# Kernel optimization log

Hardware: AMD Instinct MI355X
Metric: run time of the kernel (lower is better)

The kernel has to match this reference:

```python
import jax, jax.numpy as jnp
import numpy as np

B, T, H, W, C = 8, 16, 64, 64, 16
HID = 64  # hidden_dim of each ConvLSTM cell
K = 3     # kernel size


def _convlstm_step(x, h, c, Wk, b):
    # conv over concat([x, h]) -> 4*HID gate channels (i, f, o, g)
    z = jax.lax.conv_general_dilated(
        jnp.concatenate([x, h], axis=-1), Wk,
        window_strides=(1, 1), padding='SAME',
        dimension_numbers=('NHWC', 'HWIO', 'NHWC')) + b
    i, f, o, g = jnp.split(z, 4, axis=-1)
    c_new = jax.nn.sigmoid(f) * c + jax.nn.sigmoid(i) * jnp.tanh(g)
    h_new = jax.nn.sigmoid(o) * jnp.tanh(c_new)
    return h_new, c_new


def setup_inputs() -> dict:
    key = jax.random.key(0)
    k1, k2, k3 = jax.random.split(key, 3)
    enc_input = jax.random.normal(k1, (B, T, H, W, C), jnp.float32)
    # input cell: in_channels = C + HID; stacked hidden cell: 2*HID
    W0 = jax.random.normal(k2, (K, K, C + HID, 4 * HID), jnp.float32) * 0.05
    b0 = jnp.zeros((4 * HID,), jnp.float32)
    W1 = jax.random.normal(k3, (K, K, 2 * HID, 4 * HID), jnp.float32) * 0.05
    b1 = jnp.zeros((4 * HID,), jnp.float32)
    return {"enc_input": enc_input, "W0": W0, "b0": b0, "W1": W1, "b1": b1}


def reference(enc_input, W0, b0, W1, b1):
    Bv, Tv, Hv, Wv, _ = enc_input.shape
    z0 = jnp.zeros((Bv, Hv, Wv, HID), enc_input.dtype)

    def step(carry, x_t):
        h0, c0, h1, c1 = carry
        h0, c0 = _convlstm_step(x_t, h0, c0, W0, b0)   # input ConvLSTM
        h1, c1 = _convlstm_step(h0, h1, c1, W1, b1)    # stacked hidden ConvLSTM
        return (h0, c0, h1, c1), None

    xs = jnp.moveaxis(enc_input, 1, 0)  # [T, B, H, W, C]
    (h0, c0, h1, c1), _ = jax.lax.scan(step, (z0, z0, z0, z0), xs)
    # Encoder returns last hidden layer's (h, c)
    return (h1, c1)
```

## Files before the change

kernel.cpp:

```cpp
#include <hip/hip_runtime.h>
#include <hip/hip_bf16.h>

#define Bv 8
#define Tv 16
#define Hv 64
#define Wv 64
#define Cv 16
#define HID 64
#define PH 66

typedef short short8 __attribute__((ext_vector_type(8)));
typedef float f32x4 __attribute__((ext_vector_type(4)));
typedef unsigned short u16x8 __attribute__((ext_vector_type(8)));

__device__ __forceinline__ unsigned short f2bf(float x) {
  union { float f; unsigned int u; } v; v.f = x;
  unsigned int r = v.u + 0x7FFF + ((v.u >> 16) & 1);
  return (unsigned short)(r >> 16);
}
__device__ __forceinline__ float sigmoid_f(float x) {
  return 1.f / (1.f + __expf(-x));
}
__device__ __forceinline__ float tanh_f(float x) {
  float e = __expf(2.f * x);
  return 1.f - 2.f / (e + 1.f);
}

__global__ void relayout_w0(const float* __restrict__ W0, unsigned short* __restrict__ out) {
  int o = blockIdx.x * 256 + threadIdx.x;
  if (o >= 27 * 8192) return;
  int cc = o >> 13, t = o & 8191;
  int wn = t >> 11, t2 = t & 2047;
  int g = t2 >> 9, t3 = t2 & 511;
  int l = t3 >> 3, e = t3 & 7;
  int kg = l >> 4, r = l & 15;
  int k = kg * 8 + e;
  int col = g * 64 + wn * 16 + r;
  int tap = cc / 3, cgi = cc - tap * 3;
  int p = cgi * 32 + k;
  float v = 0.f;
  if (p < 16)        v = W0[(size_t)(tap * 80 + p) * 256 + col];
  else if (p >= 32)  v = W0[(size_t)(tap * 80 + (p - 16)) * 256 + col];
  out[o] = f2bf(v);
}
__global__ void relayout_w1(const float* __restrict__ W1, unsigned short* __restrict__ out) {
  int o = blockIdx.x * 256 + threadIdx.x;
  if (o >= 36 * 8192) return;
  int cc = o >> 13, t = o & 8191;
  int wn = t >> 11, t2 = t & 2047;
  int g = t2 >> 9, t3 = t2 & 511;
  int l = t3 >> 3, e = t3 & 7;
  int kg = l >> 4, r = l & 15;
  int k = kg * 8 + e;
  int col = g * 64 + wn * 16 + r;
  int tap = cc >> 2, cgi = cc & 3;
  out[o] = f2bf(W1[(size_t)(tap * 128 + cgi * 32 + k) * 256 + col]);
}

__global__ void zero_init(unsigned short* __restrict__ h0a, unsigned short* __restrict__ h0b,
                          unsigned short* __restrict__ h1a, unsigned short* __restrict__ h1b,
                          unsigned short* __restrict__ xb) {
  int idx = blockIdx.x * 256 + threadIdx.x;
  u16x8 z = {};
  const int XB_CH = (Bv * PH * PH * 32 * 2 * 2) / 16;
  if (idx < XB_CH) { *(u16x8*)(xb + idx * 8) = z; return; }
  idx -= XB_CH;
  int bufi = idx / 16640;
  if (bufi >= 4) return;
  int rem = idx - bufi * 16640;
  int b = rem / 2080, r2 = rem - b * 2080;
  int hp = r2 >> 3, c8 = r2 & 7;
  int y, x;
  if (hp < 66)       { y = 0;  x = hp; }
  else if (hp < 132) { y = 65; x = hp - 66; }
  else { int i2 = hp - 132; y = 1 + (i2 >> 1); x = (i2 & 1) * 65; }
  unsigned short* base = (bufi == 0) ? h0a : (bufi == 1) ? h0b : (bufi == 2) ? h1a : h1b;
  *(u16x8*)(base + ((size_t)((b * PH + y) * PH) + x) * 64 + c8 * 8) = z;
}

__global__ void convert_x0(const float* __restrict__ enc, unsigned short* __restrict__ xb) {
  int idx = blockIdx.x * 256 + threadIdx.x;
  int b = idx >> 12, pix = idx & 4095;
  int y = pix >> 6, x = pix & 63;
  const float* s = enc + ((size_t)(b * Tv + 0) * 4096 + pix) * 16;
  float4 f0 = *(const float4*)(s);
  float4 f1 = *(const float4*)(s + 4);
  float4 f2 = *(const float4*)(s + 8);
  float4 f3 = *(const float4*)(s + 12);
  u16x8 o0, o1;
  o0[0]=f2bf(f0.x); o0[1]=f2bf(f0.y); o0[2]=f2bf(f0.z); o0[3]=f2bf(f0.w);
  o0[4]=f2bf(f1.x); o0[5]=f2bf(f1.y); o0[6]=f2bf(f1.z); o0[7]=f2bf(f1.w);
  o1[0]=f2bf(f2.x); o1[1]=f2bf(f2.y); o1[2]=f2bf(f2.z); o1[3]=f2bf(f2.w);
  o1[4]=f2bf(f3.x); o1[5]=f2bf(f3.y); o1[6]=f2bf(f3.z); o1[7]=f2bf(f3.w);
  unsigned short* d = xb + ((size_t)((b * PH + y + 1) * PH) + (x + 1)) * 32;
  *(u16x8*)(d)     = o0;
  *(u16x8*)(d + 8) = o1;
}

template<int CELL, int NC>
__device__ __forceinline__ void cell_run(
    const char* __restrict__ A0, const char* __restrict__ A1,
    const char* __restrict__ Wr, const float* __restrict__ bias,
    float* __restrict__ cbuf, unsigned short* __restrict__ hout,
    float* __restrict__ h1fin, float* __restrict__ c1fin,
    char* lds, int b, int by, int bx, int tid)
{
  constexpr bool T0C = (CELL == 0) ? (NC == 9) : (NC == 18);
  const int l = tid & 63, w = tid >> 6;
  const int wm = w >> 2, wn = w & 3;
  const int r = l & 15, kg = l >> 4;
  const int j = wn * 16 + r;

  int pixs;
  {
    int ps = w * 16 + r;
    int ys = by * 16 + (ps >> 3), xs = bx * 8 + (ps & 7);
    pixs = (b * PH + ys) * PH + xs;
  }

  auto ISSUE = [&](int cc, int buf) {
    char* dst = lds + buf * 24576;
    int tap, cgi, wcc;
    if (CELL == 0) {
      if (T0C) { tap = cc; cgi = 0; wcc = cc * 3; }
      else     { tap = cc / 3; cgi = cc - tap * 3; wcc = cc; }
    } else {
      if (T0C) { tap = cc >> 1; cgi = cc & 1; wcc = tap * 4 + cgi; }
      else     { tap = cc >> 2; cgi = cc & 3; wcc = cc; }
    }
    int ky = tap / 3, kx = tap - ky * 3;
    const char* srcb;
    unsigned aoff;
    if (CELL == 0) {
      if (cgi == 0) { srcb = A0; aoff = (unsigned)((pixs + ky * PH + kx) * 64 + kg * 16); }
      else { srcb = A1;
             aoff = (unsigned)((pixs + ky * PH + kx) * 128 + ((cgi == 2) ? 64 : 0) + kg * 16); }
    } else {
      srcb = (cgi < 2) ? A0 : A1;
      aoff = (unsigned)((pixs + ky * PH + kx) * 128 + (cgi & 1) * 64 + kg * 16);
    }
    __builtin_amdgcn_global_load_lds((const unsigned int*)(srcb + aoff),
                                     (unsigned int*)(dst + w * 1024), 16, 0, 0);
    const char* wp = Wr + (size_t)wcc * 16384 + (unsigned)(w * 2048 + l * 16);
    __builtin_amdgcn_global_load_lds((const unsigned int*)(wp),
                                     (unsigned int*)(dst + 8192 + w * 2048), 16, 0, 0);
    __builtin_amdgcn_global_load_lds((const unsigned int*)(wp + 1024),
                                     (unsigned int*)(dst + 8192 + w * 2048 + 1024), 16, 0, 0);
  };

  f32x4 acc[4][4] = {};
  short8 af[4], bfv[4];

  ISSUE(0, 0); ISSUE(1, 1);
#pragma unroll
  for (int cc = 0; cc < NC; ++cc) {
    if (cc <= NC - 2) { asm volatile("s_waitcnt vmcnt(3)" ::: "memory"); }
    else              { asm volatile("s_waitcnt vmcnt(0)" ::: "memory"); }
    __builtin_amdgcn_sched_barrier(0);
    __builtin_amdgcn_s_barrier();
    __builtin_amdgcn_sched_barrier(0);

    const char* bufp = lds + (cc % 3) * 24576;
#pragma unroll
    for (int mi = 0; mi < 4; ++mi)
      af[mi] = *(const short8*)(bufp + (wm * 4 + mi) * 1024 + l * 16);
#pragma unroll
    for (int g = 0; g < 4; ++g)
      bfv[g] = *(const short8*)(bufp + 8192 + (wn * 4 + g) * 1024 + l * 16);

    asm volatile("s_waitcnt lgkmcnt(0)" ::: "memory");
    __builtin_amdgcn_sched_barrier(0);
    if (cc + 2 < NC) ISSUE(cc + 2, (cc + 2) % 3);
    __builtin_amdgcn_sched_barrier(0);

#pragma unroll
    for (int mi = 0; mi < 4; ++mi)
#pragma unroll
      for (int g = 0; g < 4; ++g)
        acc[mi][g] = __builtin_amdgcn_mfma_f32_16x16x32_bf16(
            af[mi], bfv[g], acc[mi][g], 0, 0, 0);
  }

  float bi[4];
#pragma unroll
  for (int g = 0; g < 4; ++g) bi[g] = bias[g * 64 + j];
  float cpre[4][4];
#pragma unroll
  for (int mi = 0; mi < 4; ++mi) {
#pragma unroll
    for (int rg = 0; rg < 4; ++rg) {
      if constexpr (T0C) { cpre[mi][rg] = 0.f; }
      else {
        int p = wm * 64 + mi * 16 + kg * 4 + rg;
        int y = by * 16 + (p >> 3), x = bx * 8 + (p & 7);
        cpre[mi][rg] = cbuf[((size_t)((b * Hv + y) * Wv) + x) * HID + j];
      }
    }
  }
#pragma unroll
  for (int mi = 0; mi < 4; ++mi) {
#pragma unroll
    for (int rg = 0; rg < 4; ++rg) {
      int p = wm * 64 + mi * 16 + kg * 4 + rg;
      int y = by * 16 + (p >> 3), x = bx * 8 + (p & 7);
      float zi = acc[mi][0][rg] + bi[0];
      float zf = acc[mi][1][rg] + bi[1];
      float zo = acc[mi][2][rg] + bi[2];
      float zg = acc[mi][3][rg] + bi[3];
      float cn = sigmoid_f(zf) * cpre[mi][rg] + sigmoid_f(zi) * tanh_f(zg);
      float hn = sigmoid_f(zo) * tanh_f(cn);
      size_t ci = ((size_t)((b * Hv + y) * Wv) + x) * HID + j;
      cbuf[ci] = cn;
      hout[((size_t)((b * PH + y + 1) * PH) + (x + 1)) * HID + j] = f2bf(hn);
      if (CELL == 1 && h1fin != nullptr) {
        h1fin[ci] = hn;
        c1fin[ci] = cn;
      }
    }
  }
}

template<int NC1, int NC0, bool LAST>
__global__ __launch_bounds__(512, 4)
void step_fused(const unsigned short* __restrict__ xbr, unsigned short* __restrict__ xbw,
                const unsigned short* __restrict__ h0r, unsigned short* __restrict__ h0w,
                const unsigned short* __restrict__ h1r, unsigned short* __restrict__ h1w,
                const unsigned short* __restrict__ w0r, const unsigned short* __restrict__ w1r,
                const float* __restrict__ b0, const float* __restrict__ b1,
                float* __restrict__ c0, float* __restrict__ c1,
                float* __restrict__ h1f, float* __restrict__ c1f,
                const float* __restrict__ enc, int tnext)
{
  extern __shared__ char lds[];
  const int tid = threadIdx.x;
  const int gid = blockIdx.x;
  int isC1, k;
  if constexpr (NC1 > 0 && NC0 > 0) { isC1 = gid & 1; k = gid >> 1; }
  else if constexpr (NC1 > 0)       { isC1 = 1; k = gid; }
  else                              { isC1 = 0; k = gid; }
  const int b = k >> 5, rem = k & 31;
  const int by = rem >> 3, bx = rem & 7;

  if constexpr (NC1 > 0) {
    if (isC1) {
      cell_run<1, NC1>((const char*)h0r, (const char*)h1r, (const char*)w1r, b1,
                       c1, h1w, LAST ? h1f : nullptr, LAST ? c1f : nullptr,
                       lds, b, by, bx, tid);
      return;
    }
  }
  if constexpr (NC0 > 0) {
    cell_run<0, NC0>((const char*)xbr, (const char*)h0r, (const char*)w0r, b0,
                     c0, h0w, nullptr, nullptr, lds, b, by, bx, tid);
    if (tnext >= 0) {
      int pp = tid >> 2, q4 = tid & 3;
      int y = by * 16 + (pp >> 3), x = bx * 8 + (pp & 7);
      const float* s = enc + ((size_t)(b * Tv + tnext) * 4096 + (y * 64 + x)) * 16 + q4 * 4;
      float4 f = *(const float4*)s;
      unsigned short* d = xbw + ((size_t)((b * PH + y + 1) * PH) + (x + 1)) * 32 + q4 * 4;
      d[0] = f2bf(f.x); d[1] = f2bf(f.y); d[2] = f2bf(f.z); d[3] = f2bf(f.w);
    }
  }
}

extern "C" void kernel_launch(void* const* d_in, const int* in_sizes, int n_in,
                              void* d_out, int out_size, void* d_ws, size_t ws_size,
                              hipStream_t stream) {
  const float* enc = (const float*)d_in[0];
  const float* W0  = (const float*)d_in[1];
  const float* b0  = (const float*)d_in[2];
  const float* W1  = (const float*)d_in[3];
  const float* b1  = (const float*)d_in[4];

  float* out = (float*)d_out;
  const size_t NST = (size_t)Bv * Hv * Wv * HID;
  float* h1f = out;
  float* c1  = out + NST;

  char* ws = (char*)d_ws;
  const size_t SZ_C = NST * 4;
  const size_t SZ_H = (size_t)Bv * PH * PH * HID * 2;
  const size_t SZ_X = (size_t)Bv * PH * PH * 32 * 2;
  float*          c0  = (float*)ws;
  unsigned short* h0a = (unsigned short*)(ws + SZ_C);
  unsigned short* h0b = (unsigned short*)(ws + SZ_C + SZ_H);
  unsigned short* h1a = (unsigned short*)(ws + SZ_C + 2 * SZ_H);
  unsigned short* h1b = (unsigned short*)(ws + SZ_C + 3 * SZ_H);
  unsigned short* xb0 = (unsigned short*)(ws + SZ_C + 4 * SZ_H);
  unsigned short* xb1 = (unsigned short*)(ws + SZ_C + 4 * SZ_H + SZ_X);
  unsigned short* w0r = (unsigned short*)(ws + SZ_C + 4 * SZ_H + 2 * SZ_X);
  unsigned short* w1r = (unsigned short*)(ws + SZ_C + 4 * SZ_H + 2 * SZ_X + (size_t)27 * 16384);

  hipFuncSetAttribute((const void*)step_fused<0,9,false>,   hipFuncAttributeMaxDynamicSharedMemorySize, 73728);
  hipFuncSetAttribute((const void*)step_fused<18,27,false>, hipFuncAttributeMaxDynamicSharedMemorySize, 73728);
  hipFuncSetAttribute((const void*)step_fused<36,27,false>, hipFuncAttributeMaxDynamicSharedMemorySize, 73728);
  hipFuncSetAttribute((const void*)step_fused<36,0,true>,   hipFuncAttributeMaxDynamicSharedMemorySize, 73728);

  zero_init<<<1349, 256, 0, stream>>>(h0a, h0b, h1a, h1b, xb0);
  relayout_w0<<<864, 256, 0, stream>>>(W0, w0r);
  relayout_w1<<<1152, 256, 0, stream>>>(W1, w1r);
  convert_x0<<<128, 256, 0, stream>>>(enc, xb0);

  const int LDSB = 73728;
  step_fused<0,9,false><<<256, 512, LDSB, stream>>>(
      xb0, xb1, h0b, h0a, h1a, h1b, w0r, w1r, b0, b1, c0, c1,
      nullptr, nullptr, enc, 1);
  for (int t = 1; t <= 15; ++t) {
    unsigned short* h0r = (t & 1) ? h0a : h0b;
    unsigned short* h0w = (t & 1) ? h0b : h0a;
    unsigned short* h1r = (t & 1) ? h1b : h1a;
    unsigned short* h1w = (t & 1) ? h1a : h1b;
    unsigned short* xr  = (t & 1) ? xb1 : xb0;
    unsigned short* xw  = (t & 1) ? xb0 : xb1;
    int tn = (t + 1 <= 15) ? (t + 1) : -1;
    if (t == 1)
      step_fused<18,27,false><<<512, 512, LDSB, stream>>>(
          xr, xw, h0r, h0w, h1r, h1w, w0r, w1r, b0, b1, c0, c1,
          nullptr, nullptr, enc, tn);
    else
      step_fused<36,27,false><<<512, 512, LDSB, stream>>>(
          xr, xw, h0r, h0w, h1r, h1w, w0r, w1r, b0, b1, c0, c1,
          nullptr, nullptr, enc, tn);
  }
  step_fused<36,0,true><<<256, 512, LDSB, stream>>>(
      xb0, xb1, h0b, h0a, h1a, h1b, w0r, w1r, b0, b1, c0, c1,
      h1f, c1, enc, -1);
}
```

Measured before the change: 671.8 us.

## Pack x input channels two taps per K-chunk and drop zero padding in cell 0

The x buffer shrinks from 32 to 16 channels per pixel. Cell 0 now packs two conv taps of the 16 x channels into each 32-wide K chunk, so the layer-0 reduction falls from 27 to 23 chunks (5 for x plus 18 for h). The weight relayout is rewritten to match, and the ninth tap's empty half reads from a zero pad pixel. The next chunk's issue also moves ahead of the LDS fragment reads, and the explicit lgkmcnt wait goes away, to overlap global loads with LDS reads. This relies on the barrier to keep the buffer being refilled from colliding with the one being read.

Result: faster. 649.1 us (-3.4%).

```diff
diff --git a/kernel.cpp b/kernel.cpp
--- a/kernel.cpp
+++ b/kernel.cpp
@@ -26,23 +26,6 @@
   return 1.f - 2.f / (e + 1.f);
 }
 
-__global__ void relayout_w0(const float* __restrict__ W0, unsigned short* __restrict__ out) {
-  int o = blockIdx.x * 256 + threadIdx.x;
-  if (o >= 27 * 8192) return;
-  int cc = o >> 13, t = o & 8191;
-  int wn = t >> 11, t2 = t & 2047;
-  int g = t2 >> 9, t3 = t2 & 511;
-  int l = t3 >> 3, e = t3 & 7;
-  int kg = l >> 4, r = l & 15;
-  int k = kg * 8 + e;
-  int col = g * 64 + wn * 16 + r;
-  int tap = cc / 3, cgi = cc - tap * 3;
-  int p = cgi * 32 + k;
-  float v = 0.f;
-  if (p < 16)        v = W0[(size_t)(tap * 80 + p) * 256 + col];
-  else if (p >= 32)  v = W0[(size_t)(tap * 80 + (p - 16)) * 256 + col];
-  out[o] = f2bf(v);
-}
 __global__ void relayout_w1(const float* __restrict__ W1, unsigned short* __restrict__ out) {
   int o = blockIdx.x * 256 + threadIdx.x;
   if (o >= 36 * 8192) return;
@@ -57,12 +40,35 @@
   out[o] = f2bf(W1[(size_t)(tap * 128 + cgi * 32 + k) * 256 + col]);
 }
 
+__global__ void relayout_w0(const float* __restrict__ W0, unsigned short* __restrict__ out) {
+  int o = blockIdx.x * 256 + threadIdx.x;
+  if (o >= 23 * 8192) return;
+  int cc = o >> 13, t = o & 8191;
+  int wn = t >> 11, t2 = t & 2047;
+  int g = t2 >> 9, t3 = t2 & 511;
+  int l = t3 >> 3, e = t3 & 7;
+  int kg = l >> 4, r = l & 15;
+  int k = kg * 8 + e;
+  int col = g * 64 + wn * 16 + r;
+  float v = 0.f;
+  if (cc < 4) {
+    int tap = 2 * cc + (k >> 4);
+    v = W0[(size_t)(tap * 80 + (k & 15)) * 256 + col];
+  } else if (cc == 4) {
+    if (k < 16) v = W0[(size_t)(8 * 80 + k) * 256 + col];
+  } else {
+    int hcc = cc - 5, tap = hcc >> 1, cgi = hcc & 1;
+    v = W0[(size_t)(tap * 80 + 16 + cgi * 32 + k) * 256 + col];
+  }
+  out[o] = f2bf(v);
+}
+
 __global__ void zero_init(unsigned short* __restrict__ h0a, unsigned short* __restrict__ h0b,
                           unsigned short* __restrict__ h1a, unsigned short* __restrict__ h1b,
                           unsigned short* __restrict__ xb) {
   int idx = blockIdx.x * 256 + threadIdx.x;
   u16x8 z = {};
-  const int XB_CH = (Bv * PH * PH * 32 * 2 * 2) / 16;
+  const int XB_CH = (Bv * PH * PH * 16 * 2 * 2) / 16;
   if (idx < XB_CH) { *(u16x8*)(xb + idx * 8) = z; return; }
   idx -= XB_CH;
   int bufi = idx / 16640;
@@ -92,7 +98,7 @@
   o0[4]=f2bf(f1.x); o0[5]=f2bf(f1.y); o0[6]=f2bf(f1.z); o0[7]=f2bf(f1.w);
   o1[0]=f2bf(f2.x); o1[1]=f2bf(f2.y); o1[2]=f2bf(f2.z); o1[3]=f2bf(f2.w);
   o1[4]=f2bf(f3.x); o1[5]=f2bf(f3.y); o1[6]=f2bf(f3.z); o1[7]=f2bf(f3.w);
-  unsigned short* d = xb + ((size_t)((b * PH + y + 1) * PH) + (x + 1)) * 32;
+  unsigned short* d = xb + ((size_t)((b * PH + y + 1) * PH) + (x + 1)) * 16;
   *(u16x8*)(d)     = o0;
   *(u16x8*)(d + 8) = o1;
 }
@@ -105,7 +111,7 @@
     float* __restrict__ h1fin, float* __restrict__ c1fin,
     char* lds, int b, int by, int bx, int tid)
 {
-  constexpr bool T0C = (CELL == 0) ? (NC == 9) : (NC == 18);
+  constexpr bool T0C = (CELL == 0) ? (NC == 5) : (NC == 18);
   const int l = tid & 63, w = tid >> 6;
   const int wm = w >> 2, wn = w & 3;
   const int r = l & 15, kg = l >> 4;
@@ -117,30 +123,46 @@
     int ys = by * 16 + (ps >> 3), xs = bx * 8 + (ps & 7);
     pixs = (b * PH + ys) * PH + xs;
   }
+  const int zpix = b * PH * PH;
 
   auto ISSUE = [&](int cc, int buf) {
     char* dst = lds + buf * 24576;
-    int tap, cgi, wcc;
-    if (CELL == 0) {
-      if (T0C) { tap = cc; cgi = 0; wcc = cc * 3; }
-      else     { tap = cc / 3; cgi = cc - tap * 3; wcc = cc; }
+    if constexpr (CELL == 0) {
+      if (cc < 5) {
+        int tapA = 2 * cc;
+        int kyA = tapA / 3, kxA = tapA - kyA * 3;
+        unsigned offA = (unsigned)((pixs + kyA * PH + kxA) * 32 + kg * 16);
+        unsigned offB;
+        if (cc < 4) {
+          int tapB = tapA + 1;
+          int kyB = tapB / 3, kxB = tapB - kyB * 3;
+          offB = (unsigned)((pixs + kyB * PH + kxB) * 32 + (kg - 2) * 16);
+        } else {
+          offB = (unsigned)(zpix * 32 + (kg - 2) * 16);
+        }
+        unsigned aoff = (kg < 2) ? offA : offB;
+        __builtin_amdgcn_global_load_lds((const unsigned int*)(A0 + aoff),
+                                         (unsigned int*)(dst + w * 1024), 16, 0, 0);
+      } else {
+        int hcc = cc - 5, tap = hcc >> 1, cgi = hcc & 1;
+        int ky = tap / 3, kx = tap - ky * 3;
+        unsigned aoff = (unsigned)((pixs + ky * PH + kx) * 128 + cgi * 64 + kg * 16);
+        __builtin_amdgcn_global_load_lds((const unsigned int*)(A1 + aoff),
+                                         (unsigned int*)(dst + w * 1024), 16, 0, 0);
+      }
     } else {
-      if (T0C) { tap = cc >> 1; cgi = cc & 1; wcc = tap * 4 + cgi; }
-      else     { tap = cc >> 2; cgi = cc & 3; wcc = cc; }
-    }
-    int ky = tap / 3, kx = tap - ky * 3;
-    const char* srcb;
-    unsigned aoff;
-    if (CELL == 0) {
-      if (cgi == 0) { srcb = A0; aoff = (unsigned)((pixs + ky * PH + kx) * 64 + kg * 16); }
-      else { srcb = A1;
-             aoff = (unsigned)((pixs + ky * PH + kx) * 128 + ((cgi == 2) ? 64 : 0) + kg * 16); }
-    } else {
-      srcb = (cgi < 2) ? A0 : A1;
-      aoff = (unsigned)((pixs + ky * PH + kx) * 128 + (cgi & 1) * 64 + kg * 16);
-    }
-    __builtin_amdgcn_global_load_lds((const unsigned int*)(srcb + aoff),
-                                     (unsigned int*)(dst + w * 1024), 16, 0, 0);
+      int tap, cgi;
+      if (T0C) { tap = cc >> 1; cgi = cc & 1; }
+      else     { tap = cc >> 2; cgi = cc & 3; }
+      int ky = tap / 3, kx = tap - ky * 3;
+      const char* srcb = (cgi < 2) ? A0 : A1;
+      unsigned aoff = (unsigned)((pixs + ky * PH + kx) * 128 + (cgi & 1) * 64 + kg * 16);
+      __builtin_amdgcn_global_load_lds((const unsigned int*)(srcb + aoff),
+                                       (unsigned int*)(dst + w * 1024), 16, 0, 0);
+    }
+    int wcc;
+    if constexpr (CELL == 0) wcc = cc;
+    else                     wcc = T0C ? ((cc >> 1) * 4 + (cc & 1)) : cc;
     const char* wp = Wr + (size_t)wcc * 16384 + (unsigned)(w * 2048 + l * 16);
     __builtin_amdgcn_global_load_lds((const unsigned int*)(wp),
                                      (unsigned int*)(dst + 8192 + w * 2048), 16, 0, 0);
@@ -160,6 +182,8 @@
     __builtin_amdgcn_s_barrier();
     __builtin_amdgcn_sched_barrier(0);
 
+    if (cc + 2 < NC) ISSUE(cc + 2, (cc + 2) % 3);
+
     const char* bufp = lds + (cc % 3) * 24576;
 #pragma unroll
     for (int mi = 0; mi < 4; ++mi)
@@ -167,11 +191,6 @@
 #pragma unroll
     for (int g = 0; g < 4; ++g)
       bfv[g] = *(const short8*)(bufp + 8192 + (wn * 4 + g) * 1024 + l * 16);
-
-    asm volatile("s_waitcnt lgkmcnt(0)" ::: "memory");
-    __builtin_amdgcn_sched_barrier(0);
-    if (cc + 2 < NC) ISSUE(cc + 2, (cc + 2) % 3);
-    __builtin_amdgcn_sched_barrier(0);
 
 #pragma unroll
     for (int mi = 0; mi < 4; ++mi)
@@ -257,7 +276,7 @@
       int y = by * 16 + (pp >> 3), x = bx * 8 + (pp & 7);
       const float* s = enc + ((size_t)(b * Tv + tnext) * 4096 + (y * 64 + x)) * 16 + q4 * 4;
       float4 f = *(const float4*)s;
-      unsigned short* d = xbw + ((size_t)((b * PH + y + 1) * PH) + (x + 1)) * 32 + q4 * 4;
+      unsigned short* d = xbw + ((size_t)((b * PH + y + 1) * PH) + (x + 1)) * 16 + q4 * 4;
       d[0] = f2bf(f.x); d[1] = f2bf(f.y); d[2] = f2bf(f.z); d[3] = f2bf(f.w);
     }
   }
@@ -280,7 +299,7 @@
   char* ws = (char*)d_ws;
   const size_t SZ_C = NST * 4;
   const size_t SZ_H = (size_t)Bv * PH * PH * HID * 2;
-  const size_t SZ_X = (size_t)Bv * PH * PH * 32 * 2;
+  const size_t SZ_X = (size_t)Bv * PH * PH * 16 * 2;
   float*          c0  = (float*)ws;
   unsigned short* h0a = (unsigned short*)(ws + SZ_C);
   unsigned short* h0b = (unsigned short*)(ws + SZ_C + SZ_H);
@@ -289,20 +308,20 @@
   unsigned short* xb0 = (unsigned short*)(ws + SZ_C + 4 * SZ_H);
   unsigned short* xb1 = (unsigned short*)(ws + SZ_C + 4 * SZ_H + SZ_X);
   unsigned short* w0r = (unsigned short*)(ws + SZ_C + 4 * SZ_H + 2 * SZ_X);
-  unsigned short* w1r = (unsigned short*)(ws + SZ_C + 4 * SZ_H + 2 * SZ_X + (size_t)27 * 16384);
-
-  hipFuncSetAttribute((const void*)step_fused<0,9,false>,   hipFuncAttributeMaxDynamicSharedMemorySize, 73728);
-  hipFuncSetAttribute((const void*)step_fused<18,27,false>, hipFuncAttributeMaxDynamicSharedMemorySize, 73728);
-  hipFuncSetAttribute((const void*)step_fused<36,27,false>, hipFuncAttributeMaxDynamicSharedMemorySize, 73728);
+  unsigned short* w1r = (unsigned short*)(ws + SZ_C + 4 * SZ_H + 2 * SZ_X + (size_t)23 * 16384);
+
+  hipFuncSetAttribute((const void*)step_fused<0,5,false>,   hipFuncAttributeMaxDynamicSharedMemorySize, 73728);
+  hipFuncSetAttribute((const void*)step_fused<18,23,false>, hipFuncAttributeMaxDynamicSharedMemorySize, 73728);
+  hipFuncSetAttribute((const void*)step_fused<36,23,false>, hipFuncAttributeMaxDynamicSharedMemorySize, 73728);
   hipFuncSetAttribute((const void*)step_fused<36,0,true>,   hipFuncAttributeMaxDynamicSharedMemorySize, 73728);
 
-  zero_init<<<1349, 256, 0, stream>>>(h0a, h0b, h1a, h1b, xb0);
-  relayout_w0<<<864, 256, 0, stream>>>(W0, w0r);
+  zero_init<<<805, 256, 0, stream>>>(h0a, h0b, h1a, h1b, xb0);
+  relayout_w0<<<736, 256, 0, stream>>>(W0, w0r);
   relayout_w1<<<1152, 256, 0, stream>>>(W1, w1r);
   convert_x0<<<128, 256, 0, stream>>>(enc, xb0);
 
   const int LDSB = 73728;
-  step_fused<0,9,false><<<256, 512, LDSB, stream>>>(
+  step_fused<0,5,false><<<256, 512, LDSB, stream>>>(
       xb0, xb1, h0b, h0a, h1a, h1b, w0r, w1r, b0, b1, c0, c1,
       nullptr, nullptr, enc, 1);
   for (int t = 1; t <= 15; ++t) {
@@ -314,11 +333,11 @@
     unsigned short* xw  = (t & 1) ? xb0 : xb1;
     int tn = (t + 1 <= 15) ? (t + 1) : -1;
     if (t == 1)
-      step_fused<18,27,false><<<512, 512, LDSB, stream>>>(
+      step_fused<18,23,false><<<512, 512, LDSB, stream>>>(
           xr, xw, h0r, h0w, h1r, h1w, w0r, w1r, b0, b1, c0, c1,
           nullptr, nullptr, enc, tn);
     else
-      step_fused<36,27,false><<<512, 512, LDSB, stream>>>(
+      step_fused<36,23,false><<<512, 512, LDSB, stream>>>(
           xr, xw, h0r, h0w, h1r, h1w, w0r, w1r, b0, b1, c0, c1,
           nullptr, nullptr, enc, tn);
   }
```
